# Optimization experiments

Hardware: AMD Instinct MI355X
Metric: run time of the kernel (lower is better)

The kernel has to match this reference:

```python
import jax, jax.numpy as jnp
import numpy as np

B, C2D, C3D, H, W, N = 4, 64, 64, 256, 256, 16384
NEG_SLOPE = 0.1


def _conv1x1_lrelu(x, w, b):
    # 1x1 conv (no norm) + leaky_relu(0.1), per Conv2dNormRelu defaults
    y = jnp.einsum('bchw,oc->bohw', x, w) + b[None, :, None, None]
    return jax.nn.leaky_relu(y, NEG_SLOPE)


def _batch_gather(feat, idx):
    # feat: [B, C, N], idx: [B, P] -> [B, C, P]
    return jnp.take_along_axis(feat, idx[:, None, :], axis=2)


def setup_inputs() -> dict:
    key = jax.random.key(0)
    ks = jax.random.split(key, 14)
    f = jax.random.normal
    s = 0.05
    return {
        'xy': jax.random.uniform(ks[0], (B, 2, N), jnp.float32) * jnp.float32(W),
        'feat_2d': f(ks[1], (B, C2D, H, W), jnp.float32),
        'feat_3d': f(ks[2], (B, C3D, N), jnp.float32),
        'last_flow_2d': f(ks[3], (B, 2, H, W), jnp.float32),
        'last_flow_3d_to_2d': f(ks[4], (B, 2, N), jnp.float32),
        'nn_proj': jax.random.randint(ks[5], (B, H, W, 1), 0, N, jnp.int32),
        'w1': f(ks[6], (C3D, C3D + 5), jnp.float32) * s,
        'b1': f(ks[7], (C3D,), jnp.float32) * s,
        'w2': f(ks[8], (C3D, C3D), jnp.float32) * s,
        'b2': f(ks[9], (C3D,), jnp.float32) * s,
        'w3': f(ks[10], (C3D, C3D), jnp.float32) * s,
        'b3': f(ks[11], (C3D,), jnp.float32) * s,
        'wf': f(ks[12], (C2D, C2D + C3D), jnp.float32) * s,
        'bf': f(ks[13], (C2D,), jnp.float32) * s,
    }


def reference(xy, feat_2d, feat_3d, last_flow_2d, last_flow_3d_to_2d, nn_proj,
              w1, b1, w2, b2, w3, b3, wf, bf):
    b, _, h, w = feat_2d.shape
    # concat per-point flow onto 3D features: [B, C3D+2, N]
    feat_3d_aug = jnp.concatenate([feat_3d, last_flow_3d_to_2d], axis=1)

    idx = nn_proj[..., 0].reshape(b, h * w)  # nearest-neighbor point per pixel
    gathered = _batch_gather(feat_3d_aug, idx).reshape(b, -1, h, w)  # [B, C3D+2, H, W]
    xy_proj = _batch_gather(xy, idx).reshape(b, 2, h, w)             # [B, 2, H, W]

    # pixel-coordinate mesh grid: channel 0 = x (width), channel 1 = y (height)
    gy, gx = jnp.meshgrid(jnp.arange(h, dtype=xy.dtype), jnp.arange(w, dtype=xy.dtype), indexing='ij')
    grid = jnp.stack([gx, gy], axis=0)[None]  # [1, 2, H, W]
    offset = xy_proj - grid                    # [B, 2, H, W]

    # correlation between gathered 3D feats and 2D feats (channel mean)
    corr = jnp.mean(gathered[:, :C2D] * feat_2d, axis=1, keepdims=True)  # [B, 1, H, W]

    # last 2 channels are the projected flow; subtract detached last_flow_2d
    flow_ch = gathered[:, -2:] - jax.lax.stop_gradient(last_flow_2d)
    x = jnp.concatenate([corr, offset, gathered[:, :-2], flow_ch], axis=1)  # [B, C3D+5, H, W]

    x = _conv1x1_lrelu(x, w1, b1)
    x = _conv1x1_lrelu(x, w2, b2)
    x = _conv1x1_lrelu(x, w3, b3)
    out = _conv1x1_lrelu(jnp.concatenate([x, feat_2d], axis=1), wf, bf)  # [B, C2D, H, W]
    return out
```

## Files before the change

### kernel.cpp

```cpp
#include <hip/hip_runtime.h>

#define BB 4
#define CH 64
#define HW 65536
#define NN 16384
#define NT 128
#define XPITCH 72
#define LPITCH 72
#define F2PITCH 72
#define W1OFS 0
#define W2OFS 4096
#define W3OFS 8192
#define WFOFS 12288
#define FWS_BYTE 46080
#define PTAB_BYTE 49152
#define PT_ROW 160
#define WS_NEED ((size_t)PTAB_BYTE + (size_t)BB * NN * PT_ROW)

typedef __attribute__((ext_vector_type(8))) short short8;
typedef __attribute__((ext_vector_type(4))) float f32x4;

union frag_u { unsigned short u[8]; short8 v; };
union row_u  { uint4 q[4]; unsigned short u[32]; };
union half_u { uint4 q[2]; unsigned short u[16]; };

static __device__ __forceinline__ unsigned short f2bf(float x) {
    unsigned int u = __float_as_uint(x);
    return (unsigned short)((u + 0x7fffu + ((u >> 16) & 1u)) >> 16);
}
static __device__ __forceinline__ float bf2f(unsigned short h) {
    return __uint_as_float(((unsigned int)h) << 16);
}

__global__ __launch_bounds__(256) void prep(
    const float* __restrict__ xy, const float* __restrict__ f3d,
    const float* __restrict__ lf3d,
    const float* __restrict__ w1, const float* __restrict__ b1,
    const float* __restrict__ w2, const float* __restrict__ b2,
    const float* __restrict__ w3, const float* __restrict__ b3,
    const float* __restrict__ wf, const float* __restrict__ bf,
    unsigned short* __restrict__ wpk, float* __restrict__ fws,
    char* __restrict__ pt)
{
    const int t = threadIdx.x;
    const int bx = blockIdx.x;
    if (bx >= NN / 64) {
        if (blockIdx.y != 0) return;
        const int blk = bx - NN / 64;
        if (blk == 0) {
            for (int i = t; i < 64 * 64; i += 256) {
                const int m = i >> 6, k = i & 63;
                wpk[W1OFS + i] = f2bf(w1[m * 69 + 3 + k]);
            }
        } else if (blk == 1) {
            for (int i = t; i < 64 * 64; i += 256) wpk[W2OFS + i] = f2bf(w2[i]);
        } else if (blk == 2) {
            for (int i = t; i < 64 * 64; i += 256) wpk[W3OFS + i] = f2bf(w3[i]);
        } else if (blk == 3) {
            for (int i = t; i < 64 * 128; i += 256) wpk[WFOFS + i] = f2bf(wf[i]);
        } else if (t < 64) {
            fws[t]       = b1[t];
            fws[64 + t]  = b2[t];
            fws[128 + t] = b3[t];
            fws[192 + t] = bf[t];
            fws[256 + t] = w1[t * 69 + 1];
            fws[320 + t] = w1[t * 69 + 2];
            fws[384 + t] = w1[t * 69 + 0];
            fws[448 + t] = w1[t * 69 + 67];
            fws[512 + t] = w1[t * 69 + 68];
        }
        return;
    }
    const int cq = t >> 6;
    const int l = t & 63;
    const int gn = bx * 64 + l;
    const int b = blockIdx.y;
    half_u r;
#pragma unroll
    for (int i = 0; i < 16; i++)
        r.u[i] = f2bf(f3d[(size_t)(b * CH + cq * 16 + i) * NN + gn]);
    char* row = pt + ((size_t)b * NN + gn) * PT_ROW;
    uint4* rq = (uint4*)row;
    rq[2 * cq] = r.q[0];
    rq[2 * cq + 1] = r.q[1];
    if (cq == 0) {
        float4 e;
        e.x = xy[(size_t)(b * 2 + 0) * NN + gn];
        e.y = xy[(size_t)(b * 2 + 1) * NN + gn];
        e.z = lf3d[(size_t)(b * 2 + 0) * NN + gn];
        e.w = lf3d[(size_t)(b * 2 + 1) * NN + gn];
        *(float4*)(row + 144) = e;
    }
}

template<int KT, int KROW, bool LO>
static __device__ __forceinline__ void layer_mfma(
    const unsigned short* __restrict__ wrow,
    const unsigned short* Xh, const unsigned short* Xl,
    int w, int ln, int q, f32x4 acc[4][2])
{
#pragma unroll
    for (int kt = 0; kt < KT; kt++) {
        const int kcol = kt * 32 + q * 8;
        short8 A[4];
#pragma unroll
        for (int mi = 0; mi < 4; mi++)
            A[mi] = *(const short8*)(wrow + (mi * 16 + ln) * KROW + kcol);
#pragma unroll
        for (int ni = 0; ni < 2; ni++) {
            const int nr = 32 * w + ni * 16 + ln;
            short8 bh = *(const short8*)(Xh + nr * XPITCH + kcol);
            short8 bl = bh;
            if (LO) bl = *(const short8*)(Xl + nr * LPITCH + kcol);
#pragma unroll
            for (int mi = 0; mi < 4; mi++) {
                acc[mi][ni] = __builtin_amdgcn_mfma_f32_16x16x32_bf16(A[mi], bh, acc[mi][ni], 0, 0, 0);
                if (LO)
                    acc[mi][ni] = __builtin_amdgcn_mfma_f32_16x16x32_bf16(A[mi], bl, acc[mi][ni], 0, 0, 0);
            }
        }
    }
}

static __device__ __forceinline__ void zero_acc(f32x4 acc[4][2]) {
#pragma unroll
    for (int mi = 0; mi < 4; mi++)
#pragma unroll
        for (int ni = 0; ni < 2; ni++)
#pragma unroll
            for (int r = 0; r < 4; r++) acc[mi][ni][r] = 0.f;
}

static __device__ __forceinline__ void epi_x(
    f32x4 acc[4][2], const float* __restrict__ fws, int bofs, bool off_fix,
    const float* offsp, const float* auxp, unsigned short* Xh, unsigned short* Xl,
    int w, int ln, int q)
{
#pragma unroll
    for (int mi = 0; mi < 4; mi++) {
        const float4 bias = *(const float4*)(fws + bofs + mi * 16 + q * 4);
        float4 wox = bias, woy = bias, wco = bias, wfx = bias, wfy = bias;
        if (off_fix) {
            wox = *(const float4*)(fws + 256 + mi * 16 + q * 4);
            woy = *(const float4*)(fws + 320 + mi * 16 + q * 4);
            wco = *(const float4*)(fws + 384 + mi * 16 + q * 4);
            wfx = *(const float4*)(fws + 448 + mi * 16 + q * 4);
            wfy = *(const float4*)(fws + 512 + mi * 16 + q * 4);
        }
#pragma unroll
        for (int ni = 0; ni < 2; ni++) {
            const int nr = 32 * w + ni * 16 + ln;
            float ox = 0.f, oy = 0.f, co = 0.f, fx = 0.f, fy = 0.f;
            if (off_fix) {
                ox = offsp[nr]; oy = offsp[NT + nr];
                co = auxp[nr];  fx = auxp[NT + nr]; fy = auxp[2 * NT + nr];
            }
            unsigned int hh0 = 0, hh1 = 0, ll0 = 0, ll1 = 0;
#pragma unroll
            for (int r = 0; r < 4; r++) {
                float a = acc[mi][ni][r] + ((const float*)&bias)[r];
                if (off_fix) {
                    a += ((const float*)&wox)[r] * ox + ((const float*)&woy)[r] * oy;
                    a += ((const float*)&wco)[r] * co;
                    a += ((const float*)&wfx)[r] * fx + ((const float*)&wfy)[r] * fy;
                }
                a = fmaxf(a, 0.1f * a);
                const unsigned short hb = f2bf(a);
                const unsigned short lb = f2bf(a - bf2f(hb));
                if (r == 0) { hh0 = hb; ll0 = lb; }
                if (r == 1) { hh0 |= ((unsigned)hb) << 16; ll0 |= ((unsigned)lb) << 16; }
                if (r == 2) { hh1 = hb; ll1 = lb; }
                if (r == 3) { hh1 |= ((unsigned)hb) << 16; ll1 |= ((unsigned)lb) << 16; }
            }
            *(uint2*)&Xh[nr * XPITCH + mi * 16 + q * 4] = make_uint2(hh0, hh1);
            *(uint2*)&Xl[nr * LPITCH + mi * 16 + q * 4] = make_uint2(ll0, ll1);
        }
    }
}

__global__ __launch_bounds__(256, 2) void fuse(
    const float* __restrict__ feat2d, const float* __restrict__ lf2d,
    const int* __restrict__ nn,
    const unsigned short* __restrict__ wpk, const float* __restrict__ fws,
    const char* __restrict__ ptab,
    float* __restrict__ out)
{
    __shared__ unsigned short Xhi[NT * XPITCH];
    __shared__ unsigned short Xlo[NT * LPITCH];
    __shared__ unsigned short F2[NT * F2PITCH];
    __shared__ float offsS[2 * NT];
    __shared__ float auxS[3 * NT];

    const int tid = threadIdx.x;
    const int w = tid >> 6, lane = tid & 63;
    const int q = lane >> 4, ln = lane & 15;
    const int b = blockIdx.y;
    const int p0 = blockIdx.x * NT;

    {
        const int ci = lane >> 3;
        const int qd = lane & 7;
        const int px0 = 32 * w + qd * 4;
        float4 fv[8];
#pragma unroll
        for (int cc = 0; cc < 8; cc++) {
            const int c = ci * 8 + cc;
            fv[cc] = *(const float4*)(feat2d + (size_t)(b * CH + c) * HW + p0 + px0);
        }
#pragma unroll
        for (int px = 0; px < 4; px++) {
            frag_u fr;
#pragma unroll
            for (int cc = 0; cc < 8; cc++)
                fr.u[cc] = f2bf(((const float*)&fv[cc])[px]);
            *(short8*)&F2[(px0 + px) * F2PITCH + ci * 8] = fr.v;
        }
    }

    {
        const int cp = lane >> 5, j = lane & 31;
        const int n = 32 * w + j;
        const int p = p0 + n;
        const int idx = nn[(size_t)b * HW + p];
        const char* prow = ptab + ((size_t)b * NN + idx) * PT_ROW;
        row_u g;
#pragma unroll
        for (int k = 0; k < 4; k++) g.q[k] = ((const uint4*)prow)[cp * 4 + k];
        uint4* xp = (uint4*)&Xhi[n * XPITCH + cp * 32];
#pragma unroll
        for (int k = 0; k < 4; k++) xp[k] = g.q[k];
        frag_u f2v[4];
#pragma unroll
        for (int k = 0; k < 4; k++)
            f2v[k].v = *(const short8*)&F2[n * F2PITCH + cp * 32 + k * 8];
        float ca = 0.f;
#pragma unroll
        for (int i = 0; i < 32; i++)
            ca += bf2f(f2v[i >> 3].u[i & 7]) * bf2f(g.u[i]);
        ca += __shfl_xor(ca, 32);
        if (cp == 0) {
            const float4 e = *(const float4*)(prow + 144);
            offsS[n] = e.x - (float)(p & 255);
            offsS[NT + n] = e.y - (float)(p >> 8);
            auxS[n] = ca * (1.0f / 64.0f);
            auxS[NT + n] = e.z - lf2d[(size_t)(b * 2 + 0) * HW + p];
            auxS[2 * NT + n] = e.w - lf2d[(size_t)(b * 2 + 1) * HW + p];
        }
    }

    f32x4 acc[4][2];
    zero_acc(acc);
    layer_mfma<2, 64, false>(wpk + W1OFS, Xhi, Xlo, w, ln, q, acc);
    epi_x(acc, fws, 0, true, offsS, auxS, Xhi, Xlo, w, ln, q);
    zero_acc(acc);
    layer_mfma<2, 64, true>(wpk + W2OFS, Xhi, Xlo, w, ln, q, acc);
    epi_x(acc, fws, 64, false, offsS, auxS, Xhi, Xlo, w, ln, q);
    zero_acc(acc);
    layer_mfma<2, 64, true>(wpk + W3OFS, Xhi, Xlo, w, ln, q, acc);
    epi_x(acc, fws, 128, false, offsS, auxS, Xhi, Xlo, w, ln, q);
    zero_acc(acc);
    layer_mfma<2, 128, true>(wpk + WFOFS, Xhi, Xlo, w, ln, q, acc);
#pragma unroll
    for (int kt = 2; kt < 4; kt++) {
        const int kcol = kt * 32 + q * 8;
        short8 A[4];
#pragma unroll
        for (int mi = 0; mi < 4; mi++)
            A[mi] = *(const short8*)(wpk + WFOFS + (mi * 16 + ln) * 128 + kcol);
#pragma unroll
        for (int ni = 0; ni < 2; ni++) {
            const int nr = 32 * w + ni * 16 + ln;
            frag_u fh;
            fh.v = *(const short8*)&F2[nr * F2PITCH + (kt - 2) * 32 + q * 8];
#pragma unroll
            for (int mi = 0; mi < 4; mi++)
                acc[mi][ni] = __builtin_amdgcn_mfma_f32_16x16x32_bf16(A[mi], fh.v, acc[mi][ni], 0, 0, 0);
        }
    }
#pragma unroll
    for (int mi = 0; mi < 4; mi++) {
        const float4 bias = *(const float4*)(fws + 192 + mi * 16 + q * 4);
#pragma unroll
        for (int ni = 0; ni < 2; ni++) {
#pragma unroll
            for (int r = 0; r < 4; r++) {
                float a = acc[mi][ni][r] + ((const float*)&bias)[r];
                a = fmaxf(a, 0.1f * a);
                const int m = mi * 16 + q * 4 + r;
                out[(size_t)(b * CH + m) * HW + p0 + 32 * w + ni * 16 + ln] = a;
            }
        }
    }
}

__global__ __launch_bounds__(256) void fuse_slow(
    const float* __restrict__ feat2d, const float* __restrict__ lf2d,
    const float* __restrict__ xy, const float* __restrict__ feat3d,
    const float* __restrict__ lf3d, const int* __restrict__ nn,
    const float* __restrict__ w1, const float* __restrict__ b1,
    const float* __restrict__ w2, const float* __restrict__ b2,
    const float* __restrict__ w3, const float* __restrict__ b3,
    const float* __restrict__ wf, const float* __restrict__ bfv,
    float* __restrict__ out)
{
    const int p = blockIdx.x * 256 + threadIdx.x;
    const int b = blockIdx.y;
    const int idx = nn[(size_t)b * HW + p];
    const float* f3 = feat3d + (size_t)b * CH * NN + idx;
    float g[CH];
#pragma unroll
    for (int c = 0; c < CH; c++) g[c] = f3[(size_t)c * NN];
    const float fl3x = lf3d[(size_t)(b * 2 + 0) * NN + idx];
    const float fl3y = lf3d[(size_t)(b * 2 + 1) * NN + idx];
    const float xyx = xy[(size_t)(b * 2 + 0) * NN + idx];
    const float xyy = xy[(size_t)(b * 2 + 1) * NN + idx];
    const float* f2p = feat2d + (size_t)b * CH * HW + p;
    float corr = 0.f;
#pragma unroll
    for (int c = 0; c < CH; c++) corr += f2p[(size_t)c * HW] * g[c];
    corr *= (1.f / 64.f);
    float xin[69];
    xin[0] = corr;
    xin[1] = xyx - (float)(p & 255);
    xin[2] = xyy - (float)(p >> 8);
#pragma unroll
    for (int c = 0; c < CH; c++) xin[3 + c] = g[c];
    xin[67] = fl3x - lf2d[(size_t)(b * 2 + 0) * HW + p];
    xin[68] = fl3y - lf2d[(size_t)(b * 2 + 1) * HW + p];
    float x1[64], x2[64], x3[64], accv[64];
#pragma unroll
    for (int o = 0; o < 64; o++) {
        float a = b1[o];
#pragma unroll
        for (int k = 0; k < 69; k++) a += w1[o * 69 + k] * xin[k];
        x1[o] = (a >= 0.f) ? a : 0.1f * a;
    }
#pragma unroll
    for (int o = 0; o < 64; o++) {
        float a = b2[o];
#pragma unroll
        for (int k = 0; k < 64; k++) a += w2[o * 64 + k] * x1[k];
        x2[o] = (a >= 0.f) ? a : 0.1f * a;
    }
#pragma unroll
    for (int o = 0; o < 64; o++) {
        float a = b3[o];
#pragma unroll
        for (int k = 0; k < 64; k++) a += w3[o * 64 + k] * x2[k];
        x3[o] = (a >= 0.f) ? a : 0.1f * a;
    }
#pragma unroll
    for (int o = 0; o < 64; o++) {
        float a = bfv[o];
#pragma unroll
        for (int k = 0; k < 64; k++) a += wf[o * 128 + k] * x3[k];
        accv[o] = a;
    }
#pragma unroll
    for (int k = 0; k < 64; k++) {
        const float f = f2p[(size_t)k * HW];
#pragma unroll
        for (int o = 0; o < 64; o++) accv[o] += wf[o * 128 + 64 + k] * f;
    }
#pragma unroll
    for (int o = 0; o < 64; o++) {
        float a = accv[o];
        a = (a >= 0.f) ? a : 0.1f * a;
        out[(size_t)(b * CH + o) * HW + p] = a;
    }
}

extern "C" void kernel_launch(void* const* d_in, const int* in_sizes, int n_in,
                              void* d_out, int out_size, void* d_ws, size_t ws_size,
                              hipStream_t stream)
{
    const float* xy   = (const float*)d_in[0];
    const float* f2d  = (const float*)d_in[1];
    const float* f3d  = (const float*)d_in[2];
    const float* lf2d = (const float*)d_in[3];
    const float* lf3d = (const float*)d_in[4];
    const int*   nn   = (const int*)d_in[5];
    const float* w1 = (const float*)d_in[6];
    const float* b1 = (const float*)d_in[7];
    const float* w2 = (const float*)d_in[8];
    const float* b2 = (const float*)d_in[9];
    const float* w3 = (const float*)d_in[10];
    const float* b3 = (const float*)d_in[11];
    const float* wf = (const float*)d_in[12];
    const float* bf = (const float*)d_in[13];

    if (ws_size >= WS_NEED) {
        unsigned short* wpk = (unsigned short*)d_ws;
        float* fws = (float*)((char*)d_ws + FWS_BYTE);
        char* pt = (char*)d_ws + PTAB_BYTE;
        prep<<<dim3(NN / 64 + 5, BB), 256, 0, stream>>>(xy, f3d, lf3d,
                                                        w1, b1, w2, b2, w3, b3, wf, bf,
                                                        wpk, fws, pt);
        fuse<<<dim3(HW / NT, BB), 256, 0, stream>>>(f2d, lf2d, nn, wpk, fws, pt, (float*)d_out);
    } else {
        fuse_slow<<<dim3(HW / 256, BB), 256, 0, stream>>>(f2d, lf2d, xy, f3d, lf3d, nn,
                                                          w1, b1, w2, b2, w3, b3, wf, bf,
                                                          (float*)d_out);
    }
}
```

Baseline: 219.9 us.

## Process two pixel tiles per block with register prefetch of the second tile

Each block now handles two 128-pixel tiles instead of one. The second tile's feat_2d, gathered point-table rows and flow values are loaded into registers before the first tile's MLP chain runs, so global-memory latency overlaps the MFMA work. The per-tile staging, correlation and compute code is split into helper functions, and the grid is halved to match. About fifty extra registers stay live across the compute phase, which risks spills or lower occupancy, and having fewer blocks reduces parallelism.

```diff
diff --git a/kernel.cpp b/kernel.cpp
--- a/kernel.cpp
+++ b/kernel.cpp
@@ -5,6 +5,7 @@
 #define HW 65536
 #define NN 16384
 #define NT 128
+#define TW 256
 #define XPITCH 72
 #define LPITCH 72
 #define F2PITCH 72
@@ -93,6 +94,79 @@
     }
 }
 
+struct pref_t {
+    float4 fv[8];
+    row_u g;
+    float4 e;
+    float lfx, lfy;
+};
+
+static __device__ __forceinline__ void tile_load(
+    pref_t& P, const float* __restrict__ feat2d, const float* __restrict__ lf2d,
+    const char* __restrict__ ptab, int b, int p_base, int w, int lane, int idx)
+{
+    const int ci = lane >> 3, qd = lane & 7;
+    const int px0 = 32 * w + qd * 4;
+#pragma unroll
+    for (int cc = 0; cc < 8; cc++)
+        P.fv[cc] = *(const float4*)(feat2d + (size_t)(b * CH + ci * 8 + cc) * HW + p_base + px0);
+    const int cp = lane >> 5, j = lane & 31;
+    const int n = 32 * w + j;
+    const char* prow = ptab + ((size_t)b * NN + idx) * PT_ROW;
+#pragma unroll
+    for (int k = 0; k < 4; k++) P.g.q[k] = ((const uint4*)prow)[cp * 4 + k];
+    if (cp == 0) {
+        P.e = *(const float4*)(prow + 144);
+        P.lfx = lf2d[(size_t)(b * 2 + 0) * HW + p_base + n];
+        P.lfy = lf2d[(size_t)(b * 2 + 1) * HW + p_base + n];
+    }
+}
+
+static __device__ __forceinline__ void tile_stage(
+    const pref_t& P, unsigned short* F2, unsigned short* Xhi, int w, int lane)
+{
+    const int ci = lane >> 3, qd = lane & 7;
+    const int px0 = 32 * w + qd * 4;
+#pragma unroll
+    for (int px = 0; px < 4; px++) {
+        frag_u fr;
+#pragma unroll
+        for (int cc = 0; cc < 8; cc++)
+            fr.u[cc] = f2bf(((const float*)&P.fv[cc])[px]);
+        *(short8*)&F2[(px0 + px) * F2PITCH + ci * 8] = fr.v;
+    }
+    const int cp = lane >> 5, j = lane & 31;
+    const int n = 32 * w + j;
+    uint4* xp = (uint4*)&Xhi[n * XPITCH + cp * 32];
+#pragma unroll
+    for (int k = 0; k < 4; k++) xp[k] = P.g.q[k];
+}
+
+static __device__ __forceinline__ void tile_corr(
+    const pref_t& P, const unsigned short* F2, float* offsS, float* auxS,
+    int p_base, int w, int lane)
+{
+    const int cp = lane >> 5, j = lane & 31;
+    const int n = 32 * w + j;
+    const int p = p_base + n;
+    frag_u f2v[4];
+#pragma unroll
+    for (int k = 0; k < 4; k++)
+        f2v[k].v = *(const short8*)&F2[n * F2PITCH + cp * 32 + k * 8];
+    float ca = 0.f;
+#pragma unroll
+    for (int i = 0; i < 32; i++)
+        ca += bf2f(f2v[i >> 3].u[i & 7]) * bf2f(P.g.u[i]);
+    ca += __shfl_xor(ca, 32);
+    if (cp == 0) {
+        offsS[n] = P.e.x - (float)(p & 255);
+        offsS[NT + n] = P.e.y - (float)(p >> 8);
+        auxS[n] = ca * (1.0f / 64.0f);
+        auxS[NT + n] = P.e.z - P.lfx;
+        auxS[2 * NT + n] = P.e.w - P.lfy;
+    }
+}
+
 template<int KT, int KROW, bool LO>
 static __device__ __forceinline__ void layer_mfma(
     const unsigned short* __restrict__ wrow,
@@ -178,6 +252,57 @@
     }
 }
 
+static __device__ __forceinline__ void compute_tile(
+    const unsigned short* Xhi, const unsigned short* Xlo, const unsigned short* F2,
+    const float* offsS, const float* auxS,
+    const unsigned short* __restrict__ wpk, const float* __restrict__ fws,
+    float* __restrict__ out, int b, int p_base, int w, int ln, int q)
+{
+    f32x4 acc[4][2];
+    zero_acc(acc);
+    layer_mfma<2, 64, false>(wpk + W1OFS, Xhi, Xlo, w, ln, q, acc);
+    epi_x(acc, fws, 0, true, offsS, auxS, (unsigned short*)Xhi, (unsigned short*)Xlo, w, ln, q);
+    zero_acc(acc);
+    layer_mfma<2, 64, true>(wpk + W2OFS, Xhi, Xlo, w, ln, q, acc);
+    epi_x(acc, fws, 64, false, offsS, auxS, (unsigned short*)Xhi, (unsigned short*)Xlo, w, ln, q);
+    zero_acc(acc);
+    layer_mfma<2, 64, true>(wpk + W3OFS, Xhi, Xlo, w, ln, q, acc);
+    epi_x(acc, fws, 128, false, offsS, auxS, (unsigned short*)Xhi, (unsigned short*)Xlo, w, ln, q);
+    zero_acc(acc);
+    layer_mfma<2, 128, true>(wpk + WFOFS, Xhi, Xlo, w, ln, q, acc);
+#pragma unroll
+    for (int kt = 2; kt < 4; kt++) {
+        const int kcol = kt * 32 + q * 8;
+        short8 A[4];
+#pragma unroll
+        for (int mi = 0; mi < 4; mi++)
+            A[mi] = *(const short8*)(wpk + WFOFS + (mi * 16 + ln) * 128 + kcol);
+#pragma unroll
+        for (int ni = 0; ni < 2; ni++) {
+            const int nr = 32 * w + ni * 16 + ln;
+            frag_u fh;
+            fh.v = *(const short8*)&F2[nr * F2PITCH + (kt - 2) * 32 + q * 8];
+#pragma unroll
+            for (int mi = 0; mi < 4; mi++)
+                acc[mi][ni] = __builtin_amdgcn_mfma_f32_16x16x32_bf16(A[mi], fh.v, acc[mi][ni], 0, 0, 0);
+        }
+    }
+#pragma unroll
+    for (int mi = 0; mi < 4; mi++) {
+        const float4 bias = *(const float4*)(fws + 192 + mi * 16 + q * 4);
+#pragma unroll
+        for (int ni = 0; ni < 2; ni++) {
+#pragma unroll
+            for (int r = 0; r < 4; r++) {
+                float a = acc[mi][ni][r] + ((const float*)&bias)[r];
+                a = fmaxf(a, 0.1f * a);
+                const int m = mi * 16 + q * 4 + r;
+                out[(size_t)(b * CH + m) * HW + p_base + 32 * w + ni * 16 + ln] = a;
+            }
+        }
+    }
+}
+
 __global__ __launch_bounds__(256, 2) void fuse(
     const float* __restrict__ feat2d, const float* __restrict__ lf2d,
     const int* __restrict__ nn,
@@ -195,102 +320,21 @@
     const int w = tid >> 6, lane = tid & 63;
     const int q = lane >> 4, ln = lane & 15;
     const int b = blockIdx.y;
-    const int p0 = blockIdx.x * NT;
-
-    {
-        const int ci = lane >> 3;
-        const int qd = lane & 7;
-        const int px0 = 32 * w + qd * 4;
-        float4 fv[8];
-#pragma unroll
-        for (int cc = 0; cc < 8; cc++) {
-            const int c = ci * 8 + cc;
-            fv[cc] = *(const float4*)(feat2d + (size_t)(b * CH + c) * HW + p0 + px0);
-        }
-#pragma unroll
-        for (int px = 0; px < 4; px++) {
-            frag_u fr;
-#pragma unroll
-            for (int cc = 0; cc < 8; cc++)
-                fr.u[cc] = f2bf(((const float*)&fv[cc])[px]);
-            *(short8*)&F2[(px0 + px) * F2PITCH + ci * 8] = fr.v;
-        }
-    }
-
-    {
-        const int cp = lane >> 5, j = lane & 31;
-        const int n = 32 * w + j;
-        const int p = p0 + n;
-        const int idx = nn[(size_t)b * HW + p];
-        const char* prow = ptab + ((size_t)b * NN + idx) * PT_ROW;
-        row_u g;
-#pragma unroll
-        for (int k = 0; k < 4; k++) g.q[k] = ((const uint4*)prow)[cp * 4 + k];
-        uint4* xp = (uint4*)&Xhi[n * XPITCH + cp * 32];
-#pragma unroll
-        for (int k = 0; k < 4; k++) xp[k] = g.q[k];
-        frag_u f2v[4];
-#pragma unroll
-        for (int k = 0; k < 4; k++)
-            f2v[k].v = *(const short8*)&F2[n * F2PITCH + cp * 32 + k * 8];
-        float ca = 0.f;
-#pragma unroll
-        for (int i = 0; i < 32; i++)
-            ca += bf2f(f2v[i >> 3].u[i & 7]) * bf2f(g.u[i]);
-        ca += __shfl_xor(ca, 32);
-        if (cp == 0) {
-            const float4 e = *(const float4*)(prow + 144);
-            offsS[n] = e.x - (float)(p & 255);
-            offsS[NT + n] = e.y - (float)(p >> 8);
-            auxS[n] = ca * (1.0f / 64.0f);
-            auxS[NT + n] = e.z - lf2d[(size_t)(b * 2 + 0) * HW + p];
-            auxS[2 * NT + n] = e.w - lf2d[(size_t)(b * 2 + 1) * HW + p];
-        }
-    }
-
-    f32x4 acc[4][2];
-    zero_acc(acc);
-    layer_mfma<2, 64, false>(wpk + W1OFS, Xhi, Xlo, w, ln, q, acc);
-    epi_x(acc, fws, 0, true, offsS, auxS, Xhi, Xlo, w, ln, q);
-    zero_acc(acc);
-    layer_mfma<2, 64, true>(wpk + W2OFS, Xhi, Xlo, w, ln, q, acc);
-    epi_x(acc, fws, 64, false, offsS, auxS, Xhi, Xlo, w, ln, q);
-    zero_acc(acc);
-    layer_mfma<2, 64, true>(wpk + W3OFS, Xhi, Xlo, w, ln, q, acc);
-    epi_x(acc, fws, 128, false, offsS, auxS, Xhi, Xlo, w, ln, q);
-    zero_acc(acc);
-    layer_mfma<2, 128, true>(wpk + WFOFS, Xhi, Xlo, w, ln, q, acc);
-#pragma unroll
-    for (int kt = 2; kt < 4; kt++) {
-        const int kcol = kt * 32 + q * 8;
-        short8 A[4];
-#pragma unroll
-        for (int mi = 0; mi < 4; mi++)
-            A[mi] = *(const short8*)(wpk + WFOFS + (mi * 16 + ln) * 128 + kcol);
-#pragma unroll
-        for (int ni = 0; ni < 2; ni++) {
-            const int nr = 32 * w + ni * 16 + ln;
-            frag_u fh;
-            fh.v = *(const short8*)&F2[nr * F2PITCH + (kt - 2) * 32 + q * 8];
-#pragma unroll
-            for (int mi = 0; mi < 4; mi++)
-                acc[mi][ni] = __builtin_amdgcn_mfma_f32_16x16x32_bf16(A[mi], fh.v, acc[mi][ni], 0, 0, 0);
-        }
-    }
-#pragma unroll
-    for (int mi = 0; mi < 4; mi++) {
-        const float4 bias = *(const float4*)(fws + 192 + mi * 16 + q * 4);
-#pragma unroll
-        for (int ni = 0; ni < 2; ni++) {
-#pragma unroll
-            for (int r = 0; r < 4; r++) {
-                float a = acc[mi][ni][r] + ((const float*)&bias)[r];
-                a = fmaxf(a, 0.1f * a);
-                const int m = mi * 16 + q * 4 + r;
-                out[(size_t)(b * CH + m) * HW + p0 + 32 * w + ni * 16 + ln] = a;
-            }
-        }
-    }
+    const int p0 = blockIdx.x * TW;
+    const int n = 32 * w + (lane & 31);
+
+    const int idx0 = nn[(size_t)b * HW + p0 + n];
+    const int idx1 = nn[(size_t)b * HW + p0 + NT + n];
+
+    pref_t P0, P1;
+    tile_load(P0, feat2d, lf2d, ptab, b, p0, w, lane, idx0);
+    tile_stage(P0, F2, Xhi, w, lane);
+    tile_load(P1, feat2d, lf2d, ptab, b, p0 + NT, w, lane, idx1);
+    tile_corr(P0, F2, offsS, auxS, p0, w, lane);
+    compute_tile(Xhi, Xlo, F2, offsS, auxS, wpk, fws, out, b, p0, w, ln, q);
+    tile_stage(P1, F2, Xhi, w, lane);
+    tile_corr(P1, F2, offsS, auxS, p0 + NT, w, lane);
+    compute_tile(Xhi, Xlo, F2, offsS, auxS, wpk, fws, out, b, p0 + NT, w, ln, q);
 }
 
 __global__ __launch_bounds__(256) void fuse_slow(
@@ -396,7 +440,7 @@
         prep<<<dim3(NN / 64 + 5, BB), 256, 0, stream>>>(xy, f3d, lf3d,
                                                         w1, b1, w2, b2, w3, b3, wf, bf,
                                                         wpk, fws, pt);
-        fuse<<<dim3(HW / NT, BB), 256, 0, stream>>>(f2d, lf2d, nn, wpk, fws, pt, (float*)d_out);
+        fuse<<<dim3(HW / TW, BB), 256, 0, stream>>>(f2d, lf2d, nn, wpk, fws, pt, (float*)d_out);
     } else {
         fuse_slow<<<dim3(HW / 256, BB), 256, 0, stream>>>(f2d, lf2d, xy, f3d, lf3d, nn,
                                                           w1, b1, w2, b2, w3, b3, wf, bf,
```

New measurement: 216.8 us. No clear change (-1.4%).
